# Kernel optimization log

Hardware: AMD Instinct MI355X
Metric: run time of the kernel (lower is better)

Reference implementation:

```python
import jax, jax.numpy as jnp
import numpy as np

N, E, D, H = 50000, 500000, 128, 128


def setup_inputs() -> dict:
    key = jax.random.key(0)
    ks = jax.random.split(key, 20)
    s = 0.05
    inp = {
        "node_states": jax.random.normal(ks[0], (N, D), jnp.float32),
        "edge_features": jax.random.normal(ks[1], (E, D), jnp.float32),
        "from_idx": jax.random.randint(ks[2], (E,), 0, N, dtype=jnp.int32),
        "to_idx": jax.random.randint(ks[3], (E,), 0, N, dtype=jnp.int32),
        "graph_idx": jax.random.randint(ks[4], (N,), 0, 16, dtype=jnp.int32),
        # message MLP: Linear(3D,H)-ReLU-Linear(H,H)-ReLU-Linear(H,D)
        "mW1": jax.random.normal(ks[5], (3 * D, H), jnp.float32) * s,
        "mb1": jnp.zeros((H,), jnp.float32),
        "mW2": jax.random.normal(ks[6], (H, H), jnp.float32) * s,
        "mb2": jnp.zeros((H,), jnp.float32),
        "mW3": jax.random.normal(ks[7], (H, D), jnp.float32) * s,
        "mb3": jnp.zeros((D,), jnp.float32),
    }
    # three GRU cells; W: input->gates [D,3D], U: hidden->gates [D,3D]; gate order r,z,n (torch)
    for i, g in enumerate(["g0", "g1", "g2"]):
        inp[g + "W"] = jax.random.normal(ks[8 + 2 * i], (D, 3 * D), jnp.float32) * s
        inp[g + "U"] = jax.random.normal(ks[9 + 2 * i], (D, 3 * D), jnp.float32) * s
        inp[g + "b"] = jnp.zeros((3 * D,), jnp.float32)
        inp[g + "c"] = jnp.zeros((3 * D,), jnp.float32)
    return inp


def _mlp(x, W1, b1, W2, b2, W3, b3):
    h = jax.nn.relu(x @ W1 + b1)
    h = jax.nn.relu(h @ W2 + b2)
    return h @ W3 + b3


def _gru(x, h, W, U, b, c):
    gi = x @ W + b  # [N,3D]
    gh = h @ U + c
    ir, iz, inn = jnp.split(gi, 3, axis=1)
    hr, hz, hn = jnp.split(gh, 3, axis=1)
    r = jax.nn.sigmoid(ir + hr)
    z = jax.nn.sigmoid(iz + hz)
    n = jnp.tanh(inn + r * hn)
    return (1.0 - z) * n + z * h


def reference(node_states, edge_features, from_idx, to_idx, graph_idx,
              mW1, mb1, mW2, mb2, mW3, mb3,
              g0W, g0U, g0b, g0c, g1W, g1U, g1b, g1c, g2W, g2U, g2b, g2c):
    n_nodes = node_states.shape[0]

    def prop_once(fi, ti):
        edge_in = jnp.concatenate(
            [node_states[fi], node_states[ti], edge_features], axis=1)  # [E,3D]
        edge_states = _mlp(edge_in, mW1, mb1, mW2, mb2, mW3, mb3)  # [E,D]
        return jax.ops.segment_sum(edge_states, ti, num_segments=n_nodes)

    # forward uses self.message_net for BOTH directions (reverse net unused)
    agg = prop_once(from_idx, to_idx) + prop_once(to_idx, from_idx)  # [N,D]

    h1 = _gru(node_states, agg, g0W, g0U, g0b, g0c)
    h2 = _gru(agg, h1, g1W, g1U, g1b, g1c)
    h3 = _gru(h1, h2, g2W, g2U, g2b, g2c)
    return h3
```

## Files before the change

### kernel.cpp

```cpp
#include <hip/hip_runtime.h>

typedef unsigned short u16;
typedef __attribute__((ext_vector_type(8))) short bf16x8;
typedef __attribute__((ext_vector_type(4))) float f32x4;

__device__ inline u16 f2bf(float f) {
  unsigned int u = __float_as_uint(f);
  u += 0x7fffu + ((u >> 16) & 1u);
  return (u16)(u >> 16);
}
__device__ inline float bf2f(u16 v) {
  return __uint_as_float((unsigned)v << 16);
}

__device__ inline uint4 pack8(float4 a, float4 b) {
  uint4 r;
  r.x = (unsigned)f2bf(a.x) | ((unsigned)f2bf(a.y) << 16);
  r.y = (unsigned)f2bf(a.z) | ((unsigned)f2bf(a.w) << 16);
  r.z = (unsigned)f2bf(b.x) | ((unsigned)f2bf(b.y) << 16);
  r.w = (unsigned)f2bf(b.z) | ((unsigned)f2bf(b.w) << 16);
  return r;
}

struct TransDesc {
  const float* src[9];
  u16* dst[9];
  int R[9];
  int C[9];
  int pre[10];
};

__global__ void transpose_all_kernel(TransDesc td) {
  int t = blockIdx.x * 256 + threadIdx.x;
  if (t >= td.pre[9]) return;
  int seg = 0;
  while (t >= td.pre[seg + 1]) ++seg;
  int local = t - td.pre[seg];
  int C = td.C[seg], R = td.R[seg];
  int r = local / C, c = local - r * C;
  td.dst[seg][(size_t)c * R + r] = f2bf(td.src[seg][local]);
}

__global__ void count_kernel(const int* __restrict__ fi,
                             const int* __restrict__ ti,
                             int* __restrict__ cnt, int E) {
  int e = blockIdx.x * 256 + threadIdx.x;
  if (e < E) {
    atomicAdd(&cnt[ti[e]], 1);
    atomicAdd(&cnt[fi[e]], 1);
  }
}

__global__ void scan1_kernel(const int* __restrict__ cnt,
                             int* __restrict__ partial, int N, int chunk) {
  __shared__ int sdata[256];
  int b = blockIdx.x, t = threadIdx.x;
  int base = b * chunk;
  int sum = 0;
  for (int i = t; i < chunk; i += 256) {
    int idx = base + i;
    if (idx < N) sum += cnt[idx];
  }
  sdata[t] = sum;
  __syncthreads();
  for (int s2 = 128; s2 > 0; s2 >>= 1) {
    if (t < s2) sdata[t] += sdata[t + s2];
    __syncthreads();
  }
  if (t == 0) partial[b] = sdata[0];
}

__global__ void scan2_kernel(int* __restrict__ partial) {
  __shared__ int s[256];
  int t = threadIdx.x;
  int own = partial[t];
  s[t] = own;
  __syncthreads();
  for (int d2 = 1; d2 < 256; d2 <<= 1) {
    int v = (t >= d2) ? s[t - d2] : 0;
    __syncthreads();
    s[t] += v;
    __syncthreads();
  }
  partial[t] = s[t] - own;
}

__global__ void scan3_kernel(const int* __restrict__ cnt,
                             const int* __restrict__ partialEx,
                             int* __restrict__ cursor, int N, int chunk) {
  __shared__ int s[256];
  int b = blockIdx.x, t = threadIdx.x;
  int base = b * chunk;
  int own = (t < chunk && base + t < N) ? cnt[base + t] : 0;
  s[t] = own;
  __syncthreads();
  for (int d2 = 1; d2 < 256; d2 <<= 1) {
    int v = (t >= d2) ? s[t - d2] : 0;
    __syncthreads();
    s[t] += v;
    __syncthreads();
  }
  int ex = s[t] - own + partialEx[b];
  if (t < chunk && base + t < N) cursor[base + t] = ex;
}

__global__ void slot_kernel(const int* __restrict__ fi,
                            const int* __restrict__ ti,
                            int* __restrict__ cursor, int* __restrict__ s_nbr,
                            int* __restrict__ s_eid, int* __restrict__ s_dest,
                            int E) {
  int e = blockIdx.x * 256 + threadIdx.x;
  if (e < E) {
    int f = fi[e], t2 = ti[e];
    int p0 = atomicAdd(&cursor[t2], 1);
    s_nbr[p0] = f;
    s_eid[p0] = e;
    s_dest[p0] = t2;
    int p1 = atomicAdd(&cursor[f], 1);
    s_nbr[p1] = t2;
    s_eid[p1] = e;
    s_dest[p1] = f;
  }
}

__device__ inline void stage_w_512(u16* sW, const u16* __restrict__ src,
                                   int roww, int colofs, int tid) {
  int n = tid >> 2, quarter = tid & 3;
  const u16* s = src + (size_t)n * roww + colofs + quarter * 32;
#pragma unroll
  for (int q = 0; q < 4; ++q) {
    uint4 v = *(const uint4*)(s + q * 8);
    int byte = n * 256 + ((quarter * 64 + q * 16) ^ ((n & 7) << 4));
    *(uint4*)((char*)sW + byte) = v;
  }
}

__device__ inline void mfma_pass(const u16* A, const u16* W, f32x4 acc[8],
                                 int w, int lane) {
  const int cA = lane & 15;
  const int ko = (lane >> 4) * 8;
  const int arow = 16 * w + cA;
#pragma unroll
  for (int kk = 0; kk < 4; ++kk) {
    int ka = (kk * 32 + ko) * 2;
    int sx = ka ^ ((cA & 7) << 4);
    bf16x8 a = *(const bf16x8*)((const char*)A + arow * 256 + sx);
#pragma unroll
    for (int nt = 0; nt < 8; ++nt) {
      bf16x8 bb = *(const bf16x8*)((const char*)W + (nt * 16 + cA) * 256 + sx);
      acc[nt] = __builtin_amdgcn_mfma_f32_16x16x32_bf16(a, bb, acc[nt], 0, 0, 0);
    }
  }
}

__device__ inline void write_h_lds(u16* sH, const f32x4 acc[8], int w,
                                   int lane) {
#pragma unroll
  for (int nt = 0; nt < 8; ++nt) {
    int col = nt * 16 + (lane & 15);
#pragma unroll
    for (int i = 0; i < 4; ++i) {
      int rr = 16 * w + ((lane >> 4) * 4) + i;
      *(u16*)((char*)sH + rr * 256 + ((col * 2) ^ ((rr & 7) << 4))) =
          f2bf(acc[nt][i]);
    }
  }
}

__global__ __launch_bounds__(512) void gemm1_kernel(
    const float* __restrict__ ns, const float* __restrict__ ef,
    const u16* __restrict__ Wt1, const float* __restrict__ b1,
    u16* __restrict__ Pa, u16* __restrict__ Pb, u16* __restrict__ EFm, int N,
    int E, int Nb) {
  __shared__ u16 sA[128 * 128];
  __shared__ u16 sW[128 * 128];
  const int tid = threadIdx.x;
  const int lane = tid & 63;
  const int w = tid >> 6;
  if ((int)blockIdx.x < Nb) {
    const int r0 = blockIdx.x * 128;
    {
      int row = tid >> 2, seg = tid & 3;
      int rr = r0 + row;
      if (rr >= N) rr = N - 1;
      const float4* sx = (const float4*)(ns + (size_t)rr * 128 + seg * 32);
#pragma unroll
      for (int q = 0; q < 4; ++q) {
        int byte = row * 256 + ((seg * 64 + q * 16) ^ ((row & 7) << 4));
        *(uint4*)((char*)sA + byte) = pack8(sx[q * 2], sx[q * 2 + 1]);
      }
    }
    stage_w_512(sW, Wt1, 384, 0, tid);
    __syncthreads();
    f32x4 accA[8] = {};
    mfma_pass(sA, sW, accA, w, lane);
    __syncthreads();
    stage_w_512(sW, Wt1, 384, 128, tid);
    __syncthreads();
    f32x4 accB[8] = {};
    mfma_pass(sA, sW, accB, w, lane);
#pragma unroll
    for (int nt = 0; nt < 8; ++nt) {
      int col = nt * 16 + (lane & 15);
#pragma unroll
      for (int i = 0; i < 4; ++i) {
        int rr = 16 * w + ((lane >> 4) * 4) + i;
        int row = r0 + rr;
        if (row < N) {
          Pa[(size_t)row * 128 + col] = f2bf(accA[nt][i]);
          Pb[(size_t)row * 128 + col] = f2bf(accB[nt][i]);
        }
      }
    }
  } else {
    const int r0 = (blockIdx.x - Nb) * 128;
    {
      int row = tid >> 2, seg = tid & 3;
      int rr = r0 + row;
      if (rr >= E) rr = E - 1;
      const float4* sx = (const float4*)(ef + (size_t)rr * 128 + seg * 32);
#pragma unroll
      for (int q = 0; q < 4; ++q) {
        int byte = row * 256 + ((seg * 64 + q * 16) ^ ((row & 7) << 4));
        *(uint4*)((char*)sA + byte) = pack8(sx[q * 2], sx[q * 2 + 1]);
      }
    }
    stage_w_512(sW, Wt1, 384, 256, tid);
    __syncthreads();
    f32x4 acc[8] = {};
    mfma_pass(sA, sW, acc, w, lane);
    __syncthreads();
#pragma unroll
    for (int nt = 0; nt < 8; ++nt) {
      int col = nt * 16 + (lane & 15);
      float bv = b1[col];
#pragma unroll
      for (int i = 0; i < 4; ++i) {
        int rr = 16 * w + ((lane >> 4) * 4) + i;
        *(u16*)((char*)sA + rr * 256 + ((col * 2) ^ ((rr & 7) << 4))) =
            f2bf(acc[nt][i] + bv);
      }
    }
    __syncthreads();
#pragma unroll
    for (int it = 0; it < 4; ++it) {
      int task = tid + (it << 9);
      int row = task >> 4, c8 = task & 15;
      int gr = r0 + row;
      if (gr < E) {
        uint4 v = *(const uint4*)((const char*)sA + row * 256 +
                                  ((c8 << 4) ^ ((row & 7) << 4)));
        *(uint4*)(EFm + (size_t)gr * 128 + (c8 << 3)) = v;
      }
    }
  }
}

__global__ __launch_bounds__(512, 2) void edge_csr2_kernel(
    const u16* __restrict__ EFm, const int* __restrict__ s_nbr,
    const int* __restrict__ s_eid, const int* __restrict__ s_dest,
    const u16* __restrict__ Wt2, const u16* __restrict__ Wt3,
    const u16* __restrict__ Pa, const u16* __restrict__ Pb,
    const float* __restrict__ b2, const float* __restrict__ b3,
    float* __restrict__ aggf, int nslots, int ntiles) {
  __shared__ u16 sW2[128 * 128];
  __shared__ u16 sW3[128 * 128];
  __shared__ u16 sH[64 * 128];
  const int tid = threadIdx.x;
  const int lane = tid & 63;
  const int wv = tid >> 6;
  const int mw = wv >> 1;
  const int nw = wv & 1;
  const int l15 = lane & 15;
  const int lhi = lane >> 4;

  stage_w_512(sW2, Wt2, 128, 0, tid);
  stage_w_512(sW3, Wt3, 128, 0, tid);
  float b2f[4], b3f[4];
#pragma unroll
  for (int nt = 0; nt < 4; ++nt) {
    int col = (nw << 6) + (nt << 4) + l15;
    b2f[nt] = b2[col];
    b3f[nt] = b3[col];
  }
  __syncthreads();

  const int ra = (mw << 4) + l15;

  for (int t = blockIdx.x; t < ntiles; t += gridDim.x) {
    const int r0 = t << 6;
#pragma unroll
    for (int it = 0; it < 2; ++it) {
      int task = tid + (it << 9);
      int row = task >> 4;
      int c8 = task & 15;
      int r = r0 + row;
      int rc = r < nslots ? r : nslots - 1;
      int nbr = s_nbr[rc], eid = s_eid[rc], dst = s_dest[rc];
      uint4 efv = *(const uint4*)(EFm + (size_t)eid * 128 + (c8 << 3));
      uint4 pav = *(const uint4*)(Pa + (size_t)nbr * 128 + (c8 << 3));
      uint4 pbv = *(const uint4*)(Pb + (size_t)dst * 128 + (c8 << 3));
      const u16* pe = (const u16*)&efv;
      const u16* pa = (const u16*)&pav;
      const u16* pb = (const u16*)&pbv;
      unsigned o[4];
#pragma unroll
      for (int j = 0; j < 4; ++j) {
        float v0 = fmaxf(bf2f(pe[2 * j]) + bf2f(pa[2 * j]) + bf2f(pb[2 * j]), 0.f);
        float v1 = fmaxf(bf2f(pe[2 * j + 1]) + bf2f(pa[2 * j + 1]) + bf2f(pb[2 * j + 1]), 0.f);
        o[j] = (unsigned)f2bf(v0) | ((unsigned)f2bf(v1) << 16);
      }
      *(uint4*)((char*)sH + row * 256 + ((c8 << 4) ^ ((row & 7) << 4))) = *(uint4*)o;
    }
    __syncthreads();
    bf16x8 hA[4];
#pragma unroll
    for (int kk = 0; kk < 4; ++kk) {
      int sx = ((kk << 6) + (lhi << 4)) ^ ((ra & 7) << 4);
      hA[kk] = *(const bf16x8*)((const char*)sH + ra * 256 + sx);
    }
    f32x4 acc[4] = {};
#pragma unroll
    for (int kk = 0; kk < 4; ++kk) {
#pragma unroll
      for (int nt = 0; nt < 4; ++nt) {
        int c = (nw << 6) + (nt << 4) + l15;
        int sx = ((kk << 6) + (lhi << 4)) ^ ((c & 7) << 4);
        bf16x8 bb = *(const bf16x8*)((const char*)sW2 + c * 256 + sx);
        acc[nt] = __builtin_amdgcn_mfma_f32_16x16x32_bf16(hA[kk], bb, acc[nt], 0, 0, 0);
      }
    }
    __syncthreads();
#pragma unroll
    for (int i = 0; i < 4; ++i) {
      int rl = (mw << 4) + (lhi << 2) + i;
#pragma unroll
      for (int nt = 0; nt < 4; ++nt) {
        int col = (nw << 6) + (nt << 4) + l15;
        float v = fmaxf(acc[nt][i] + b2f[nt], 0.f);
        *(u16*)((char*)sH + rl * 256 + ((col * 2) ^ ((rl & 7) << 4))) = f2bf(v);
        acc[nt][i] = 0.f;
      }
    }
    __syncthreads();
#pragma unroll
    for (int kk = 0; kk < 4; ++kk) {
      int sx = ((kk << 6) + (lhi << 4)) ^ ((ra & 7) << 4);
      hA[kk] = *(const bf16x8*)((const char*)sH + ra * 256 + sx);
    }
#pragma unroll
    for (int kk = 0; kk < 4; ++kk) {
#pragma unroll
      for (int nt = 0; nt < 4; ++nt) {
        int c = (nw << 6) + (nt << 4) + l15;
        int sx = ((kk << 6) + (lhi << 4)) ^ ((c & 7) << 4);
        bf16x8 bb = *(const bf16x8*)((const char*)sW3 + c * 256 + sx);
        acc[nt] = __builtin_amdgcn_mfma_f32_16x16x32_bf16(hA[kk], bb, acc[nt], 0, 0, 0);
      }
    }
    __syncthreads();
#pragma unroll
    for (int i = 0; i < 4; ++i) {
      int rl = (mw << 4) + (lhi << 2) + i;
#pragma unroll
      for (int nt = 0; nt < 4; ++nt) {
        int col = (nw << 6) + (nt << 4) + l15;
        *(u16*)((char*)sH + rl * 256 + ((col * 2) ^ ((rl & 7) << 4))) =
            f2bf(acc[nt][i] + b3f[nt]);
      }
    }
    __syncthreads();
    {
      int c = tid & 127, q = tid >> 7;
      float s = 0.f;
      int prev = -1;
      int rbeg = q << 4;
#pragma unroll 4
      for (int rr = rbeg; rr < rbeg + 16; ++rr) {
        int r = r0 + rr;
        int d = (r < nslots) ? s_dest[r] : -1;
        if (d != prev) {
          if (prev >= 0) unsafeAtomicAdd(&aggf[(size_t)prev * 128 + c], s);
          prev = d;
          s = 0.f;
        }
        if (d >= 0)
          s += bf2f(*(const u16*)((const char*)sH + rr * 256 +
                                  ((c * 2) ^ ((rr & 7) << 4))));
      }
      if (prev >= 0) unsafeAtomicAdd(&aggf[(size_t)prev * 128 + c], s);
    }
    __syncthreads();
  }
}

__global__ __launch_bounds__(512, 1) void gru3_kernel(
    const float* __restrict__ ns, const float* __restrict__ aggf,
    const u16* __restrict__ g0W, const u16* __restrict__ g0U,
    const u16* __restrict__ g1W, const u16* __restrict__ g1U,
    const u16* __restrict__ g2W, const u16* __restrict__ g2U,
    const float* __restrict__ b0, const float* __restrict__ c0,
    const float* __restrict__ b1, const float* __restrict__ c1,
    const float* __restrict__ b2, const float* __restrict__ c2,
    float* __restrict__ out, int N) {
  __shared__ u16 sX[128 * 128];
  __shared__ u16 sG[128 * 128];
  __shared__ u16 sW[2][128 * 128];
  const int tid = threadIdx.x;
  const int lane = tid & 63;
  const int w = tid >> 6;
  const int r0 = blockIdx.x * 128;
  {
    int row = tid >> 2, seg = tid & 3;
    int rr = r0 + row;
    if (rr >= N) rr = N - 1;
    const float4* sx = (const float4*)(ns + (size_t)rr * 128 + seg * 32);
    const float4* sh = (const float4*)(aggf + (size_t)rr * 128 + seg * 32);
#pragma unroll
    for (int q = 0; q < 4; ++q) {
      int byte = row * 256 + ((seg * 64 + q * 16) ^ ((row & 7) << 4));
      *(uint4*)((char*)sX + byte) = pack8(sx[q * 2], sx[q * 2 + 1]);
      *(uint4*)((char*)sG + byte) = pack8(sh[q * 2], sh[q * 2 + 1]);
    }
  }

  const u16* wseq[18] = {
      g0W,          g0U,          g0W + 16384, g0U + 16384, g0W + 32768, g0U + 32768,
      g1W,          g1U,          g1W + 16384, g1U + 16384, g1W + 32768, g1U + 32768,
      g2W,          g2U,          g2W + 16384, g2U + 16384, g2W + 32768, g2U + 32768};

  stage_w_512(sW[0], wseq[0], 128, 0, tid);
  __syncthreads();

  float hpf[8][4];

#define PIPE_PASS(PH, ABUF, ACC)                                    \
  {                                                                 \
    if ((PH) + 1 < 18) stage_w_512(sW[((PH) + 1) & 1], wseq[(PH) + 1], 128, 0, tid); \
    mfma_pass((ABUF), sW[(PH) & 1], (ACC), w, lane);                \
    __syncthreads();                                                \
  }

  {
    f32x4 ar[8] = {}, az[8] = {}, ai[8] = {}, ah[8] = {};
    PIPE_PASS(0, sX, ar)
    PIPE_PASS(1, sG, ar)
    PIPE_PASS(2, sX, az)
    PIPE_PASS(3, sG, az)
    PIPE_PASS(4, sX, ai)
    PIPE_PASS(5, sG, ah)
    f32x4 h1[8];
#pragma unroll
    for (int nt = 0; nt < 8; ++nt) {
      int col = nt * 16 + (lane & 15);
      float brc = b0[col] + c0[col];
      float bzc = b0[128 + col] + c0[128 + col];
      float bi = b0[256 + col];
      float bc2 = c0[256 + col];
#pragma unroll
      for (int i = 0; i < 4; ++i) {
        int rloc = 16 * w + ((lane >> 4) * 4) + i;
        int row = r0 + rloc;
        int rowc = row < N ? row : N - 1;
        float hf = aggf[(size_t)rowc * 128 + col];
        float rg = 1.f / (1.f + __expf(-(ar[nt][i] + brc)));
        float zg = 1.f / (1.f + __expf(-(az[nt][i] + bzc)));
        float pre = ai[nt][i] + bi + rg * (ah[nt][i] + bc2);
        float ng = 2.f / (1.f + __expf(-2.f * pre)) - 1.f;
        float hv = (1.f - zg) * ng + zg * hf;
        h1[nt][i] = hv;
        hpf[nt][i] = hv;
      }
    }
    write_h_lds(sX, h1, w, lane);
  }
  {
    f32x4 ar[8] = {}, az[8] = {}, ai[8] = {}, ah[8] = {};
    PIPE_PASS(6, sG, ar)
    PIPE_PASS(7, sX, ar)
    PIPE_PASS(8, sG, az)
    PIPE_PASS(9, sX, az)
    PIPE_PASS(10, sG, ai)
    PIPE_PASS(11, sX, ah)
    f32x4 h2[8];
#pragma unroll
    for (int nt = 0; nt < 8; ++nt) {
      int col = nt * 16 + (lane & 15);
      float brc = b1[col] + c1[col];
      float bzc = b1[128 + col] + c1[128 + col];
      float bi = b1[256 + col];
      float bc2 = c1[256 + col];
#pragma unroll
      for (int i = 0; i < 4; ++i) {
        float rg = 1.f / (1.f + __expf(-(ar[nt][i] + brc)));
        float zg = 1.f / (1.f + __expf(-(az[nt][i] + bzc)));
        float pre = ai[nt][i] + bi + rg * (ah[nt][i] + bc2);
        float ng = 2.f / (1.f + __expf(-2.f * pre)) - 1.f;
        float hv = (1.f - zg) * ng + zg * hpf[nt][i];
        h2[nt][i] = hv;
        hpf[nt][i] = hv;
      }
    }
    write_h_lds(sG, h2, w, lane);
  }
  {
    f32x4 ar[8] = {}, az[8] = {}, ai[8] = {}, ah[8] = {};
    PIPE_PASS(12, sX, ar)
    PIPE_PASS(13, sG, ar)
    PIPE_PASS(14, sX, az)
    PIPE_PASS(15, sG, az)
    PIPE_PASS(16, sX, ai)
    PIPE_PASS(17, sG, ah)
#pragma unroll
    for (int nt = 0; nt < 8; ++nt) {
      int col = nt * 16 + (lane & 15);
      float brc = b2[col] + c2[col];
      float bzc = b2[128 + col] + c2[128 + col];
      float bi = b2[256 + col];
      float bc2 = c2[256 + col];
#pragma unroll
      for (int i = 0; i < 4; ++i) {
        int rloc = 16 * w + ((lane >> 4) * 4) + i;
        int row = r0 + rloc;
        if (row < N) {
          float rg = 1.f / (1.f + __expf(-(ar[nt][i] + brc)));
          float zg = 1.f / (1.f + __expf(-(az[nt][i] + bzc)));
          float pre = ai[nt][i] + bi + rg * (ah[nt][i] + bc2);
          float ng = 2.f / (1.f + __expf(-2.f * pre)) - 1.f;
          out[(size_t)row * 128 + col] = (1.f - zg) * ng + zg * hpf[nt][i];
        }
      }
    }
  }
#undef PIPE_PASS
}

extern "C" void kernel_launch(void* const* d_in, const int* in_sizes, int n_in,
                              void* d_out, int out_size, void* d_ws,
                              size_t ws_size, hipStream_t stream) {
  const float* ns = (const float*)d_in[0];
  const float* ef = (const float*)d_in[1];
  const int* from_idx = (const int*)d_in[2];
  const int* to_idx = (const int*)d_in[3];
  const float* mW1 = (const float*)d_in[5];
  const float* mb1 = (const float*)d_in[6];
  const float* mW2 = (const float*)d_in[7];
  const float* mb2 = (const float*)d_in[8];
  const float* mW3 = (const float*)d_in[9];
  const float* mb3 = (const float*)d_in[10];
  const float* gW[3] = {(const float*)d_in[11], (const float*)d_in[15], (const float*)d_in[19]};
  const float* gU[3] = {(const float*)d_in[12], (const float*)d_in[16], (const float*)d_in[20]};
  const float* gb[3] = {(const float*)d_in[13], (const float*)d_in[17], (const float*)d_in[21]};
  const float* gc[3] = {(const float*)d_in[14], (const float*)d_in[18], (const float*)d_in[22]};

  const int N = in_sizes[0] / 128;
  const int E = in_sizes[1] / 128;
  const int nslots = 2 * E;

  char* base = (char*)d_ws;
  size_t cur = 0;
  auto alloc = [&](size_t bytes) {
    size_t p = cur;
    cur = (cur + bytes + 255) & ~(size_t)255;
    return (void*)(base + p);
  };
  float* aggf = (float*)alloc((size_t)N * 128 * 4);
  u16* Pa = (u16*)alloc((size_t)N * 128 * 2);
  u16* Pb = (u16*)alloc((size_t)N * 128 * 2);
  u16* Wt1 = (u16*)alloc(384 * 128 * 2);
  u16* Wt2 = (u16*)alloc(128 * 128 * 2);
  u16* Wt3 = (u16*)alloc(128 * 128 * 2);
  u16 *gWt[3], *gUt[3];
  for (int i = 0; i < 3; ++i) {
    gWt[i] = (u16*)alloc(384 * 128 * 2);
    gUt[i] = (u16*)alloc(384 * 128 * 2);
  }
  int* cnt = (int*)alloc((size_t)N * 4);
  int* cursor = (int*)alloc((size_t)N * 4);
  int* partial = (int*)alloc(256 * 4);
  int* s_nbr = (int*)alloc((size_t)nslots * 4);
  int* s_eid = (int*)alloc((size_t)nslots * 4);
  int* s_dest = (int*)alloc((size_t)nslots * 4);
  u16* EFm = (u16*)alloc((size_t)E * 128 * 2);
  (void)ws_size;

  {
    TransDesc td;
    const float* srcs[9] = {mW1, mW2, mW3, gW[0], gU[0], gW[1], gU[1], gW[2], gU[2]};
    u16* dsts[9] = {Wt1, Wt2, Wt3, gWt[0], gUt[0], gWt[1], gUt[1], gWt[2], gUt[2]};
    int Rs[9] = {384, 128, 128, 128, 128, 128, 128, 128, 128};
    int Cs[9] = {128, 128, 128, 384, 384, 384, 384, 384, 384};
    int acc = 0;
    for (int i = 0; i < 9; ++i) {
      td.src[i] = srcs[i];
      td.dst[i] = dsts[i];
      td.R[i] = Rs[i];
      td.C[i] = Cs[i];
      td.pre[i] = acc;
      acc += Rs[i] * Cs[i];
    }
    td.pre[9] = acc;
    transpose_all_kernel<<<(acc + 255) / 256, 256, 0, stream>>>(td);
  }

  hipMemsetAsync(cnt, 0, (size_t)N * 4, stream);
  count_kernel<<<(E + 255) / 256, 256, 0, stream>>>(from_idx, to_idx, cnt, E);
  int chunk = (N + 255) / 256;
  scan1_kernel<<<256, 256, 0, stream>>>(cnt, partial, N, chunk);
  scan2_kernel<<<1, 256, 0, stream>>>(partial);
  scan3_kernel<<<256, 256, 0, stream>>>(cnt, partial, cursor, N, chunk);
  slot_kernel<<<(E + 255) / 256, 256, 0, stream>>>(from_idx, to_idx, cursor,
                                                   s_nbr, s_eid, s_dest, E);

  int Nb = (N + 127) / 128, Eb = (E + 127) / 128;
  gemm1_kernel<<<Nb + Eb, 512, 0, stream>>>(ns, ef, Wt1, mb1, Pa, Pb, EFm, N,
                                            E, Nb);

  hipMemsetAsync(aggf, 0, (size_t)N * 128 * 4, stream);
  int ntiles = (nslots + 63) / 64;
  int egrid = ntiles < 512 ? ntiles : 512;
  edge_csr2_kernel<<<egrid, 512, 0, stream>>>(EFm, s_nbr, s_eid, s_dest, Wt2,
                                              Wt3, Pa, Pb, mb2, mb3, aggf,
                                              nslots, ntiles);

  int gblocks = (N + 127) / 128;
  gru3_kernel<<<gblocks, 512, 0, stream>>>(
      ns, aggf, gWt[0], gUt[0], gWt[1], gUt[1], gWt[2], gUt[2], gb[0], gc[0],
      gb[1], gc[1], gb[2], gc[2], (float*)d_out, N);
}
```

Baseline: 598.1 us.

## Restructure edge MLP kernel so each wave owns 16 rows without block barriers

The edge kernel moves from 512-thread blocks that share a 64-row tile, with many __syncthreads between layers, to 1024-thread blocks where each of 16 waves owns a private 16-row tile. Layer-1 activations are built directly in registers as MFMA A operands, and each wave computes all 128 output columns, so no block barrier is needed inside the loop. The intent is to remove synchronization stalls and let waves run their gather, MFMA and atomic phases independently. The trade-offs are higher register pressure from 8 accumulators per wave, and a grid capped at 256 blocks of 1024 threads, which may cut occupancy and per-CU shared-weight reuse.

```diff
diff --git a/kernel.cpp b/kernel.cpp
--- a/kernel.cpp
+++ b/kernel.cpp
@@ -131,6 +131,18 @@
   for (int q = 0; q < 4; ++q) {
     uint4 v = *(const uint4*)(s + q * 8);
     int byte = n * 256 + ((quarter * 64 + q * 16) ^ ((n & 7) << 4));
+    *(uint4*)((char*)sW + byte) = v;
+  }
+}
+
+__device__ inline void stage_w_1024(u16* sW, const u16* __restrict__ src,
+                                    int tid) {
+  int n = tid >> 3, part = tid & 7;
+  const u16* s = src + (size_t)n * 128 + part * 16;
+#pragma unroll
+  for (int q = 0; q < 2; ++q) {
+    uint4 v = *(const uint4*)(s + q * 8);
+    int byte = n * 256 + ((part * 32 + q * 16) ^ ((n & 7) << 4));
     *(uint4*)((char*)sW + byte) = v;
   }
 }
@@ -256,7 +268,7 @@
   }
 }
 
-__global__ __launch_bounds__(512, 2) void edge_csr2_kernel(
+__global__ __launch_bounds__(1024) void edge_wp_kernel(
     const u16* __restrict__ EFm, const int* __restrict__ s_nbr,
     const int* __restrict__ s_eid, const int* __restrict__ s_dest,
     const u16* __restrict__ Wt2, const u16* __restrict__ Wt3,
@@ -265,41 +277,40 @@
     float* __restrict__ aggf, int nslots, int ntiles) {
   __shared__ u16 sW2[128 * 128];
   __shared__ u16 sW3[128 * 128];
-  __shared__ u16 sH[64 * 128];
+  __shared__ u16 sHw[16][16 * 128];
   const int tid = threadIdx.x;
   const int lane = tid & 63;
-  const int wv = tid >> 6;
-  const int mw = wv >> 1;
-  const int nw = wv & 1;
-  const int l15 = lane & 15;
+  const int w = tid >> 6;
+  const int cA = lane & 15;
   const int lhi = lane >> 4;
 
-  stage_w_512(sW2, Wt2, 128, 0, tid);
-  stage_w_512(sW3, Wt3, 128, 0, tid);
-  float b2f[4], b3f[4];
-#pragma unroll
-  for (int nt = 0; nt < 4; ++nt) {
-    int col = (nw << 6) + (nt << 4) + l15;
+  stage_w_1024(sW2, Wt2, tid);
+  stage_w_1024(sW3, Wt3, tid);
+  float b2f[8], b3f[8];
+#pragma unroll
+  for (int nt = 0; nt < 8; ++nt) {
+    int col = (nt << 4) + cA;
     b2f[nt] = b2[col];
     b3f[nt] = b3[col];
   }
   __syncthreads();
 
-  const int ra = (mw << 4) + l15;
+  u16* myH = sHw[w];
 
   for (int t = blockIdx.x; t < ntiles; t += gridDim.x) {
-    const int r0 = t << 6;
-#pragma unroll
-    for (int it = 0; it < 2; ++it) {
-      int task = tid + (it << 9);
-      int row = task >> 4;
-      int c8 = task & 15;
-      int r = r0 + row;
-      int rc = r < nslots ? r : nslots - 1;
-      int nbr = s_nbr[rc], eid = s_eid[rc], dst = s_dest[rc];
-      uint4 efv = *(const uint4*)(EFm + (size_t)eid * 128 + (c8 << 3));
-      uint4 pav = *(const uint4*)(Pa + (size_t)nbr * 128 + (c8 << 3));
-      uint4 pbv = *(const uint4*)(Pb + (size_t)dst * 128 + (c8 << 3));
+    const int r0w = (t << 8) + (w << 4);
+    if (r0w >= nslots) continue;
+    int r = r0w + cA;
+    int rc = r < nslots ? r : nslots - 1;
+    int nbr = s_nbr[rc], eid = s_eid[rc], dst = s_dest[rc];
+
+    bf16x8 a1[4];
+#pragma unroll
+    for (int kk = 0; kk < 4; ++kk) {
+      int ofs = ((kk << 2) + lhi) << 3;
+      uint4 efv = *(const uint4*)(EFm + (size_t)eid * 128 + ofs);
+      uint4 pav = *(const uint4*)(Pa + (size_t)nbr * 128 + ofs);
+      uint4 pbv = *(const uint4*)(Pb + (size_t)dst * 128 + ofs);
       const u16* pe = (const u16*)&efv;
       const u16* pa = (const u16*)&pav;
       const u16* pb = (const u16*)&pbv;
@@ -310,87 +321,77 @@
         float v1 = fmaxf(bf2f(pe[2 * j + 1]) + bf2f(pa[2 * j + 1]) + bf2f(pb[2 * j + 1]), 0.f);
         o[j] = (unsigned)f2bf(v0) | ((unsigned)f2bf(v1) << 16);
       }
-      *(uint4*)((char*)sH + row * 256 + ((c8 << 4) ^ ((row & 7) << 4))) = *(uint4*)o;
-    }
-    __syncthreads();
-    bf16x8 hA[4];
+      a1[kk] = *(bf16x8*)o;
+    }
+    f32x4 acc[8] = {};
 #pragma unroll
     for (int kk = 0; kk < 4; ++kk) {
-      int sx = ((kk << 6) + (lhi << 4)) ^ ((ra & 7) << 4);
-      hA[kk] = *(const bf16x8*)((const char*)sH + ra * 256 + sx);
-    }
-    f32x4 acc[4] = {};
+      int sxk = (kk << 6) + (lhi << 4);
+#pragma unroll
+      for (int nt = 0; nt < 8; ++nt) {
+        int c = (nt << 4) + cA;
+        bf16x8 bb = *(const bf16x8*)((const char*)sW2 + c * 256 +
+                                     (sxk ^ ((cA & 7) << 4)));
+        acc[nt] = __builtin_amdgcn_mfma_f32_16x16x32_bf16(a1[kk], bb, acc[nt], 0, 0, 0);
+      }
+    }
+#pragma unroll
+    for (int nt = 0; nt < 8; ++nt) {
+      int col = (nt << 4) + cA;
+#pragma unroll
+      for (int i = 0; i < 4; ++i) {
+        int rr = (lhi << 2) + i;
+        float v = fmaxf(acc[nt][i] + b2f[nt], 0.f);
+        *(u16*)((char*)myH + rr * 256 + ((col * 2) ^ ((rr & 7) << 4))) = f2bf(v);
+        acc[nt][i] = 0.f;
+      }
+    }
 #pragma unroll
     for (int kk = 0; kk < 4; ++kk) {
-#pragma unroll
-      for (int nt = 0; nt < 4; ++nt) {
-        int c = (nw << 6) + (nt << 4) + l15;
-        int sx = ((kk << 6) + (lhi << 4)) ^ ((c & 7) << 4);
-        bf16x8 bb = *(const bf16x8*)((const char*)sW2 + c * 256 + sx);
-        acc[nt] = __builtin_amdgcn_mfma_f32_16x16x32_bf16(hA[kk], bb, acc[nt], 0, 0, 0);
-      }
-    }
-    __syncthreads();
-#pragma unroll
-    for (int i = 0; i < 4; ++i) {
-      int rl = (mw << 4) + (lhi << 2) + i;
-#pragma unroll
-      for (int nt = 0; nt < 4; ++nt) {
-        int col = (nw << 6) + (nt << 4) + l15;
-        float v = fmaxf(acc[nt][i] + b2f[nt], 0.f);
-        *(u16*)((char*)sH + rl * 256 + ((col * 2) ^ ((rl & 7) << 4))) = f2bf(v);
-        acc[nt][i] = 0.f;
-      }
-    }
-    __syncthreads();
+      int byte = cA * 256 + (((((kk << 2) + lhi) << 4)) ^ ((cA & 7) << 4));
+      a1[kk] = *(const bf16x8*)((const char*)myH + byte);
+    }
 #pragma unroll
     for (int kk = 0; kk < 4; ++kk) {
-      int sx = ((kk << 6) + (lhi << 4)) ^ ((ra & 7) << 4);
-      hA[kk] = *(const bf16x8*)((const char*)sH + ra * 256 + sx);
-    }
-#pragma unroll
-    for (int kk = 0; kk < 4; ++kk) {
-#pragma unroll
-      for (int nt = 0; nt < 4; ++nt) {
-        int c = (nw << 6) + (nt << 4) + l15;
-        int sx = ((kk << 6) + (lhi << 4)) ^ ((c & 7) << 4);
-        bf16x8 bb = *(const bf16x8*)((const char*)sW3 + c * 256 + sx);
-        acc[nt] = __builtin_amdgcn_mfma_f32_16x16x32_bf16(hA[kk], bb, acc[nt], 0, 0, 0);
-      }
-    }
-    __syncthreads();
-#pragma unroll
-    for (int i = 0; i < 4; ++i) {
-      int rl = (mw << 4) + (lhi << 2) + i;
-#pragma unroll
-      for (int nt = 0; nt < 4; ++nt) {
-        int col = (nw << 6) + (nt << 4) + l15;
-        *(u16*)((char*)sH + rl * 256 + ((col * 2) ^ ((rl & 7) << 4))) =
+      int sxk = (kk << 6) + (lhi << 4);
+#pragma unroll
+      for (int nt = 0; nt < 8; ++nt) {
+        int c = (nt << 4) + cA;
+        bf16x8 bb = *(const bf16x8*)((const char*)sW3 + c * 256 +
+                                     (sxk ^ ((cA & 7) << 4)));
+        acc[nt] = __builtin_amdgcn_mfma_f32_16x16x32_bf16(a1[kk], bb, acc[nt], 0, 0, 0);
+      }
+    }
+#pragma unroll
+    for (int nt = 0; nt < 8; ++nt) {
+      int col = (nt << 4) + cA;
+#pragma unroll
+      for (int i = 0; i < 4; ++i) {
+        int rr = (lhi << 2) + i;
+        *(u16*)((char*)myH + rr * 256 + ((col * 2) ^ ((rr & 7) << 4))) =
             f2bf(acc[nt][i] + b3f[nt]);
       }
     }
-    __syncthreads();
-    {
-      int c = tid & 127, q = tid >> 7;
+#pragma unroll
+    for (int half = 0; half < 2; ++half) {
+      int c = lane + (half << 6);
       float s = 0.f;
       int prev = -1;
-      int rbeg = q << 4;
 #pragma unroll 4
-      for (int rr = rbeg; rr < rbeg + 16; ++rr) {
-        int r = r0 + rr;
-        int d = (r < nslots) ? s_dest[r] : -1;
+      for (int rr = 0; rr < 16; ++rr) {
+        int rg = r0w + rr;
+        int d = (rg < nslots) ? s_dest[rg] : -1;
         if (d != prev) {
           if (prev >= 0) unsafeAtomicAdd(&aggf[(size_t)prev * 128 + c], s);
           prev = d;
           s = 0.f;
         }
         if (d >= 0)
-          s += bf2f(*(const u16*)((const char*)sH + rr * 256 +
+          s += bf2f(*(const u16*)((const char*)myH + rr * 256 +
                                   ((c * 2) ^ ((rr & 7) << 4))));
       }
       if (prev >= 0) unsafeAtomicAdd(&aggf[(size_t)prev * 128 + c], s);
     }
-    __syncthreads();
   }
 }
 
@@ -617,11 +618,11 @@
                                             E, Nb);
 
   hipMemsetAsync(aggf, 0, (size_t)N * 128 * 4, stream);
-  int ntiles = (nslots + 63) / 64;
-  int egrid = ntiles < 512 ? ntiles : 512;
-  edge_csr2_kernel<<<egrid, 512, 0, stream>>>(EFm, s_nbr, s_eid, s_dest, Wt2,
-                                              Wt3, Pa, Pb, mb2, mb3, aggf,
-                                              nslots, ntiles);
+  int ntiles = (nslots + 255) / 256;
+  int egrid = ntiles < 256 ? ntiles : 256;
+  edge_wp_kernel<<<egrid, 1024, 0, stream>>>(EFm, s_nbr, s_eid, s_dest, Wt2,
+                                             Wt3, Pa, Pb, mb2, mb3, aggf,
+                                             nslots, ntiles);
 
   int gblocks = (N + 127) / 128;
   gru3_kernel<<<gblocks, 512, 0, stream>>>(
```

New measurement: 620.9 us. 3.8% more time.
